# Kernel optimization log

Hardware: AMD Instinct MI355X
Metric: run time of the kernel (lower is better)

The kernel has to match this reference:

```python
import jax, jax.numpy as jnp
import numpy as np

B, T, C, H, N = 2, 1024, 2048, 32, 64
LAYER_ID, N_LAYERS = 12, 24
EPS = 1e-5 * 8 ** 2  # GroupNorm eps = 1e-5 * head_size_divisor**2


def setup_inputs() -> dict:
    key = jax.random.key(0)
    ks = jax.random.split(key, 16)
    nrm = lambda i, shape, s: jax.random.normal(ks[i], shape, jnp.float32) * s
    r01 = LAYER_ID / (N_LAYERS - 1)
    r1a0 = 1.0 - LAYER_ID / N_LAYERS
    ddd = (jnp.arange(C, dtype=jnp.float32) / C)[None, None, :]
    nn_ = jnp.arange(C, dtype=jnp.float32) / (C - 1)
    decay_speed = -7.0 + 5.0 * nn_ ** (0.85 + r01 ** 0.5)
    lin_s = 1.0 / float(np.sqrt(C))
    inp = dict(
        x=nrm(0, (B, T, C), 1.0),
        v_first=nrm(1, (B, T, C), 1.0),
        shift_state=jnp.zeros((B, C), jnp.float32),
        wkv_state=jnp.zeros((B, H, N, N), jnp.float32),
        x_r=1.0 - ddd ** (0.2 * r1a0),
        x_w=1.0 - ddd ** (0.9 * r1a0),
        x_k=1.0 - (ddd ** (0.9 * r1a0) + 0.4 * r01),
        x_v=1.0 - (ddd ** (0.4 * r1a0) + 0.6 * r01),
        x_a=1.0 - ddd ** (0.9 * r1a0),
        x_g=1.0 - ddd ** (0.2 * r1a0),
        w0=decay_speed[None, None, :] + 0.5,
        w1=nrm(2, (C, 64), 0.05), w2=nrm(3, (64, C), 0.1),
        a0=jnp.zeros((1, 1, C), jnp.float32),
        a1=nrm(4, (C, 64), 0.05), a2=nrm(5, (64, C), 0.1),
        v0=jnp.ones((1, 1, C), jnp.float32),
        v1=nrm(6, (C, 32), 0.05), v2=nrm(7, (32, C), 0.1),
        g1=nrm(8, (C, 128), 0.05), g2=nrm(9, (128, C), 0.1),
        k_k=jnp.full((1, 1, C), 0.85, jnp.float32),
        k_a=jnp.ones((1, 1, C), jnp.float32),
        r_k=nrm(10, (H, N), 0.02),
        W_r=nrm(11, (C, C), lin_s), W_k=nrm(12, (C, C), lin_s),
        W_v=nrm(13, (C, C), lin_s), W_o=nrm(14, (C, C), lin_s),
        ln_w=jnp.ones((C,), jnp.float32), ln_b=jnp.zeros((C,), jnp.float32),
    )
    return inp


def _forward(x, v_first, shift_state, wkv_state, x_r, x_w, x_k, x_v, x_a, x_g,
             w0, w1, w2, a0, a1, a2, v0, v1, v2, g1, g2, k_k, k_a, r_k,
             W_r, W_k, W_v, W_o, ln_w, ln_b):
    # token shift
    xx = jnp.concatenate([shift_state[:, None, :], x[:, :-1]], axis=1) - x
    xr, xw, xk, xv, xa, xg = (x + xx * m for m in (x_r, x_w, x_k, x_v, x_a, x_g))
    r = xr @ W_r
    k = xk @ W_k
    v = xv @ W_v
    # log-decay (strictly negative)
    w_log = -jax.nn.softplus(-(w0 + jnp.tanh(xw @ w1) @ w2)) - 0.5
    # residual value mixing towards layer-0 v (layer_id > 0 branch)
    v = v + (v_first - v) * jax.nn.sigmoid(v0 + xv @ v1 @ v2)
    a = jax.nn.sigmoid(a0 + xa @ a1 @ a2)
    g = jax.nn.sigmoid(xg @ g1) @ g2
    # per-head L2-normalized removal key
    kk = (k * k_k).reshape(B, T, H, N)
    kk = kk / jnp.maximum(jnp.linalg.norm(kk, axis=-1, keepdims=True), 1e-12)
    k2 = k * (1.0 + (a - 1.0) * k_a)
    # time-major [T,B,H,N] for the scan
    tm = lambda t: t.reshape(B, T, H, N).transpose(1, 0, 2, 3)
    rs, ks_, vs = tm(r), tm(k2), tm(v)
    ws = jnp.exp(tm(w_log))               # per-channel decay in (0,1)
    a_in = -kk.transpose(1, 0, 2, 3)      # removal direction
    b_in = (kk * a.reshape(B, T, H, N)).transpose(1, 0, 2, 3)
    def step(S, t):  # S: [B,H,Nv,Nk]
        r_, k_, v_, w_, a_, b_ = t
        sa = jnp.einsum('bhvk,bhk->bhv', S, a_)
        S = S * w_[:, :, None, :] \
            + jnp.einsum('bhv,bhk->bhvk', sa, b_) \
            + jnp.einsum('bhv,bhk->bhvk', v_, k_)
        return S, jnp.einsum('bhvk,bhk->bhv', S, r_)
    S_final, o = jax.lax.scan(step, wkv_state, (rs, ks_, vs, ws, a_in, b_in))
    o = o.transpose(1, 0, 2, 3)           # [B,T,H,N]
    # GroupNorm with H groups over C channels (per-head normalization)
    mu = o.mean(-1, keepdims=True)
    var = ((o - mu) ** 2).mean(-1, keepdims=True)
    on = ((o - mu) / jnp.sqrt(var + EPS)).reshape(B, T, C) * ln_w + ln_b
    # rkv bonus term
    rr, kr, vr = r.reshape(B, T, H, N), k2.reshape(B, T, H, N), v.reshape(B, T, H, N)
    bonus = ((rr * kr * r_k).sum(-1, keepdims=True) * vr).reshape(B, T, C)
    out = ((on + bonus) * g) @ W_o
    return out


def reference(x, v_first, shift_state, wkv_state, x_r, x_w, x_k, x_v, x_a, x_g,
              w0, w1, w2, a0, a1, a2, v0, v1, v2, g1, g2, k_k, k_a, r_k,
              W_r, W_k, W_v, W_o, ln_w, ln_b):
    return _forward(x, v_first, shift_state, wkv_state, x_r, x_w, x_k, x_v, x_a, x_g,
                    w0, w1, w2, a0, a1, a2, v0, v1, v2, g1, g2, k_k, k_a, r_k,
                    W_r, W_k, W_v, W_o, ln_w, ln_b)
```

## Files before the change

### kernel.cpp

```cpp
#include <hip/hip_runtime.h>
#include <cstdint>
#include <cstddef>


#define DI __device__ __forceinline__
static constexpr int T_ = 1024, C_ = 2048, H_ = 32;

typedef __attribute__((ext_vector_type(8))) __bf16 bf16x8;
typedef __attribute__((ext_vector_type(4))) float f32x4;
typedef __attribute__((ext_vector_type(8))) unsigned short us8v;
typedef __attribute__((ext_vector_type(4))) unsigned short us4v;
typedef __attribute__((ext_vector_type(2))) unsigned short us2v;

DI float sig_(float z) { return 1.0f / (1.0f + expf(-z)); }

DI unsigned short f2bf(float f) {
  union { float f; uint32_t u; } v; v.f = f;
  uint32_t u = v.u;
  return (unsigned short)((u + 0x7FFFu + ((u >> 16) & 1u)) >> 16);
}
DI float bf2f(unsigned short h) {
  union { uint32_t u; float f; } v; v.u = ((uint32_t)h) << 16;
  return v.f;
}

DI float dpp_xor1_add(float x) {
  int r = __builtin_amdgcn_update_dpp(0, __float_as_int(x), 0xB1, 0xF, 0xF, true);
  return x + __int_as_float(r);
}
DI float dpp_xor2_add(float x) {
  int r = __builtin_amdgcn_update_dpp(0, __float_as_int(x), 0x4E, 0xF, 0xF, true);
  return x + __int_as_float(r);
}
DI float dpp_hm_add(float x) {
  int r = __builtin_amdgcn_update_dpp(0, __float_as_int(x), 0x141, 0xF, 0xF, true);
  return x + __int_as_float(r);
}
DI float dpp_mir_add(float x) {
  int r = __builtin_amdgcn_update_dpp(0, __float_as_int(x), 0x140, 0xF, 0xF, true);
  return x + __int_as_float(r);
}

DI void gload16(const float* g, float* l) {
  __builtin_amdgcn_global_load_lds(
      (const __attribute__((address_space(1))) uint32_t*)g,
      (__attribute__((address_space(3))) uint32_t*)l, 16, 0, 0);
}
DI void gload16u(const unsigned short* g, unsigned short* l) {
  __builtin_amdgcn_global_load_lds(
      (const __attribute__((address_space(1))) uint32_t*)g,
      (__attribute__((address_space(3))) uint32_t*)l, 16, 0, 0);
}
DI void gload4(const float* g, float* l) {
  __builtin_amdgcn_global_load_lds(
      (const __attribute__((address_space(1))) uint32_t*)g,
      (__attribute__((address_space(3))) uint32_t*)l, 4, 0, 0);
}

struct TJob { const float* src; unsigned short* dh; unsigned short* dl;
              int N, K, ntn, tile_end; };
struct TJobs { TJob j[12]; };

__global__ __launch_bounds__(256) void wtrans(TJobs P) {
  __shared__ float t[64][65];
  int bx = blockIdx.x, ji = 0;
  while (ji < 11 && bx >= P.j[ji].tile_end) ++ji;
  TJob J = P.j[ji];
  int tix = bx - (ji ? P.j[ji - 1].tile_end : 0);
  int kt = tix / J.ntn, nt = tix % J.ntn;
  int k0 = kt * 64, n0 = nt * 64;
  int tid = threadIdx.x;
  #pragma unroll
  for (int p = 0; p < 16; ++p) {
    int flat = p * 256 + tid;
    int r = flat >> 6, c = flat & 63;
    int n = n0 + c;
    t[r][c] = (n < J.N && k0 + r < J.K) ? J.src[(size_t)(k0 + r) * J.N + n] : 0.0f;
  }
  __syncthreads();
  #pragma unroll
  for (int p = 0; p < 8; ++p) {
    int flat = p * 256 + tid;
    int rr = flat >> 5, cc = (flat & 31) * 2;
    if (n0 + rr < J.N && k0 + cc < J.K) {
      float w0v = t[cc][rr], w1v = t[cc + 1][rr];
      unsigned short h0 = f2bf(w0v), h1 = f2bf(w1v);
      us2v oh, ol;
      oh.x = h0; oh.y = h1;
      ol.x = f2bf(w0v - bf2f(h0));
      ol.y = f2bf(w1v - bf2f(h1));
      size_t off = (size_t)(n0 + rr) * J.K + k0 + cc;
      *(us2v*)(J.dh + off) = oh;
      *(us2v*)(J.dl + off) = ol;
    }
  }
}

struct GJob {
  const float* A; const unsigned short* Wh; const unsigned short* Wl; float* C;
  const float* mixv; const float* shift; const float* bias;
  int N, K, ntn, kbeg, kend, atomicC, aact, epi, tile_end;
};
struct GJobs { GJob j[8]; };

__global__ __launch_bounds__(256, 2) void gemm_w256(GJobs P) {
  __shared__ unsigned short Ash[128][32];
  __shared__ unsigned short Asl[128][32];
  __shared__ unsigned short Bsh[256][32];
  __shared__ unsigned short Bsl[256][32];
  int bx = blockIdx.x, ji = 0;
  while (ji < 7 && bx >= P.j[ji].tile_end) ++ji;
  GJob J = P.j[ji];
  int tix = bx - (ji ? P.j[ji - 1].tile_end : 0);
  int mt = tix / J.ntn, nt = tix % J.ntn;
  int m0 = mt * 128, n0 = nt * 256;
  int tid = threadIdx.x;
  int lane = tid & 63, wid = tid >> 6;
  int wr = wid >> 1, wc = wid & 1;
  int l15 = lane & 15, lg = lane >> 4;
  f32x4 acc[4][8] = {};

  int sr4 = tid >> 2, sk8 = (tid & 3) * 8;
  float ax[2][8], aq[2][8], amv[8];

  auto loadA = [&](int k0) {
    int kk = k0 + sk8;
    if (J.mixv) {
      *(float4*)&amv[0] = *(const float4*)(J.mixv + kk);
      *(float4*)&amv[4] = *(const float4*)(J.mixv + kk + 4);
    }
    #pragma unroll
    for (int p = 0; p < 2; ++p) {
      int m = m0 + p * 64 + sr4;
      const float* xp0 = J.A + (size_t)m * J.K + kk;
      *(float4*)&ax[p][0] = *(const float4*)xp0;
      *(float4*)&ax[p][4] = *(const float4*)(xp0 + 4);
      if (J.mixv) {
        const float* pp = ((m & (T_ - 1)) == 0)
            ? (J.shift + (size_t)(m >> 10) * C_ + kk)
            : (xp0 - C_);
        *(float4*)&aq[p][0] = *(const float4*)pp;
        *(float4*)&aq[p][4] = *(const float4*)(pp + 4);
      }
    }
  };
  auto writeA = [&]() {
    #pragma unroll
    for (int p = 0; p < 2; ++p) {
      int r = p * 64 + sr4;
      us8v oh, ol;
      #pragma unroll
      for (int q = 0; q < 8; ++q) {
        float va = ax[p][q];
        if (J.mixv) va = va + (aq[p][q] - va) * amv[q];
        if (J.aact == 1) va = tanhf(va);
        else if (J.aact == 2) va = sig_(va);
        unsigned short hq = f2bf(va);
        oh[q] = hq;
        ol[q] = f2bf(va - bf2f(hq));
      }
      int sp = ((tid & 3) ^ ((r >> 1) & 3)) * 8;
      *(us8v*)&Ash[r][sp] = oh;
      *(us8v*)&Asl[r][sp] = ol;
    }
  };
  auto stageB = [&](int k0) {
    #pragma unroll
    for (int j = 0; j < 4; ++j) {
      int r0 = wid * 64 + j * 16;
      int rdst = r0 + (lane >> 2);
      int nrow = n0 + rdst;
      if (nrow >= J.N) nrow = J.N - 1;
      int ssrc = (lane & 3) ^ ((rdst >> 1) & 3);
      size_t gofs = (size_t)nrow * J.K + k0 + ssrc * 8;
      gload16u(J.Wh + gofs, &Bsh[r0][0]);
      gload16u(J.Wl + gofs, &Bsl[r0][0]);
    }
  };

  loadA(J.kbeg);
  stageB(J.kbeg);
  writeA();
  asm volatile("s_waitcnt vmcnt(0)" ::: "memory");
  __syncthreads();

  for (int k0 = J.kbeg; k0 < J.kend; k0 += 32) {
    bool more = (k0 + 32 < J.kend);
    if (more) loadA(k0 + 32);
    bf16x8 afh[4], afl[4];
    #pragma unroll
    for (int i = 0; i < 4; ++i) {
      int rr = wr * 64 + i * 16 + l15;
      int sa_ = (lg ^ ((rr >> 1) & 3)) * 8;
      afh[i] = __builtin_bit_cast(bf16x8, *(const us8v*)&Ash[rr][sa_]);
      afl[i] = __builtin_bit_cast(bf16x8, *(const us8v*)&Asl[rr][sa_]);
    }
    #pragma unroll
    for (int jn = 0; jn < 8; ++jn) {
      int rb = wc * 128 + jn * 16 + l15;
      int sl = (lg ^ ((rb >> 1) & 3)) * 8;
      bf16x8 bh = __builtin_bit_cast(bf16x8, *(const us8v*)&Bsh[rb][sl]);
      bf16x8 bl = __builtin_bit_cast(bf16x8, *(const us8v*)&Bsl[rb][sl]);
      #pragma unroll
      for (int i = 0; i < 4; ++i) {
        acc[i][jn] = __builtin_amdgcn_mfma_f32_16x16x32_bf16(afh[i], bh, acc[i][jn], 0, 0, 0);
        acc[i][jn] = __builtin_amdgcn_mfma_f32_16x16x32_bf16(afl[i], bh, acc[i][jn], 0, 0, 0);
        acc[i][jn] = __builtin_amdgcn_mfma_f32_16x16x32_bf16(afh[i], bl, acc[i][jn], 0, 0, 0);
      }
    }
    __syncthreads();
    if (more) { stageB(k0 + 32); writeA(); }
    asm volatile("s_waitcnt vmcnt(0)" ::: "memory");
    __syncthreads();
  }

  int orow0 = m0 + wr * 64 + 4 * lg;
  int ocol0 = n0 + wc * 128 + l15;
  #pragma unroll
  for (int i = 0; i < 4; ++i) {
    #pragma unroll
    for (int jn = 0; jn < 8; ++jn) {
      int col = ocol0 + jn * 16;
      if (col < J.N) {
        #pragma unroll
        for (int rr = 0; rr < 4; ++rr) {
          size_t idx = (size_t)(orow0 + i * 16 + rr) * J.N + col;
          float v = acc[i][jn][rr];
          if (J.epi == 1) v = sig_(J.bias[col] + v);
          else if (J.epi == 2) v = 0.60653065971263342f * sig_(J.bias[col] + v);
          if (J.atomicC)          atomicAdd(&J.C[idx], v);
          else if (J.epi == 3)    ((unsigned short*)J.C)[idx] = f2bf(v);
          else                    J.C[idx] = v;
        }
      }
    }
  }
}

__global__ __launch_bounds__(256) void prescan(
    float* __restrict__ kio, float* __restrict__ vio,
    float* __restrict__ amat_ain, float* __restrict__ vmix_bin,
    const float* __restrict__ vfirst,
    const float* __restrict__ k_k, const float* __restrict__ k_a) {
  int gh = blockIdx.x * 4 + (threadIdx.x >> 6);
  int lane = threadIdx.x & 63;
  int h = gh & (H_ - 1);
  size_t base = (size_t)gh * 64 + lane;
  int cc = h * 64 + lane;
  float kv = kio[base];
  float kkv = kv * k_k[cc];
  float ss = kkv * kkv;
  ss += __shfl_xor(ss, 1);  ss += __shfl_xor(ss, 2);  ss += __shfl_xor(ss, 4);
  ss += __shfl_xor(ss, 8);  ss += __shfl_xor(ss, 16); ss += __shfl_xor(ss, 32);
  float nrm = fmaxf(sqrtf(ss), 1e-12f);
  float kkn = kkv / nrm;
  float av = amat_ain[base];
  float vmv = vmix_bin[base];
  float vv = vio[base];
  kio[base] = kv * (1.0f + (av - 1.0f) * k_a[cc]);
  vio[base] = vv + (vfirst[base] - vv) * vmv;
  amat_ain[base] = -kkn;
  vmix_bin[base] = kkn * av;
}

static constexpr int CH = 8;
static constexpr int SEG = 512, WU = 96;

#define LOADSTEP(BUF, S_, Aa, Ww, Kk, Bb, Rr, Vt)                  \
  {                                                                \
    *(float4*)&Aa[0] = *(const float4*)&lds[BUF][3][S_][kb];       \
    *(float4*)&Ww[0] = *(const float4*)&lds[BUF][2][S_][kb];       \
    *(float4*)&Kk[0] = *(const float4*)&lds[BUF][1][S_][kb];       \
    *(float4*)&Bb[0] = *(const float4*)&lds[BUF][4][S_][kb];       \
    *(float4*)&Rr[0] = *(const float4*)&lds[BUF][0][S_][kb];       \
    Vt = vtl[BUF][S_][vr];                                         \
  }

#define COMPSTEP(Aa, Ww, Kk, Bb, Rr, Vt, TIDX)                              \
  {                                                                         \
    float p0 = S[0] * Aa[0], p1 = S[1] * Aa[1];                             \
    p0 = fmaf(S[2], Aa[2], p0);                                             \
    p1 = fmaf(S[3], Aa[3], p1);                                             \
    float sa = p0 + p1;                                                     \
    sa = dpp_xor1_add(sa);                                                  \
    sa = dpp_xor2_add(sa);                                                  \
    sa = dpp_hm_add(sa);                                                    \
    sa = dpp_mir_add(sa);                                                   \
    S[0] = fmaf(S[0], Ww[0], fmaf(Vt, Kk[0], sa * Bb[0]));                  \
    S[1] = fmaf(S[1], Ww[1], fmaf(Vt, Kk[1], sa * Bb[1]));                  \
    S[2] = fmaf(S[2], Ww[2], fmaf(Vt, Kk[2], sa * Bb[2]));                  \
    S[3] = fmaf(S[3], Ww[3], fmaf(Vt, Kk[3], sa * Bb[3]));                  \
    float y0 = S[0] * Rr[0], y1 = S[1] * Rr[1];                             \
    y0 = fmaf(S[2], Rr[2], y0);                                             \
    y1 = fmaf(S[3], Rr[3], y1);                                             \
    float y = y0 + y1;                                                      \
    y = dpp_xor1_add(y);                                                    \
    y = dpp_xor2_add(y);                                                    \
    y = dpp_hm_add(y);                                                      \
    y = dpp_mir_add(y);                                                     \
    if (kq == 0 && (TIDX) >= outfrom)                                       \
      obf[bh + (size_t)(TIDX)*2048 + v0 + vr] = f2bf(y);                    \
  }

__global__ __launch_bounds__(128) void wkv_scan_v8(
    const float* __restrict__ r, const float* __restrict__ k2,
    const float* __restrict__ w, const float* __restrict__ ain,
    const float* __restrict__ bin, const float* __restrict__ vp,
    const float* __restrict__ sInit, unsigned short* __restrict__ obf) {
  __shared__ float lds[2][5][CH][64];
  __shared__ float vtl[2][CH][8];
  int D = blockIdx.x;
  int chain = (D & 7) + 8 * (D >> 7);
  int inner = (D >> 3) & 15;
  int seg = inner >> 3, vpair = inner & 7;
  int b = chain >> 5, h = chain & 31;
  int v0 = vpair * 8;
  int tid = threadIdx.x;
  int wid = tid >> 6, lane = tid & 63;
  int vl = lane >> 4, kq = lane & 15;
  int kb = kq * 4;
  int vr = wid * 4 + vl;
  size_t bh = (size_t)(b * T_) * 2048 + (size_t)h * 64;

  float S[4];
  if (seg == 0) {
    const float* sp = sInit + (((size_t)chain * 64 + v0 + vr) * 64) + kb;
    float4 s0 = *(const float4*)sp;
    S[0] = s0.x; S[1] = s0.y; S[2] = s0.z; S[3] = s0.w;
  } else {
    S[0] = S[1] = S[2] = S[3] = 0.0f;
  }

  const float* arr[5] = {r, k2, w, ain, bin};

  auto stage = [&](int buf, int t0) {
    for (int d = wid; d < 10; d += 2) {
      int a = d >> 1, hf = d & 1;
      size_t gofs = bh + (size_t)(t0 + hf * 4 + (lane >> 4)) * 2048 + (lane & 15) * 4;
      gload16(arr[a] + gofs, &lds[buf][a][hf * 4][0]);
    }
    if (wid == 0) {
      size_t gofs = bh + (size_t)(t0 + (lane >> 3)) * 2048 + v0 + (lane & 7);
      gload4(vp + gofs, &vtl[buf][0][0]);
    }
  };

  int tstart = seg ? (SEG - WU) : 0;
  int nch = (seg ? (SEG + WU) : SEG) / CH;
  int outfrom = seg * SEG;

  stage(0, tstart);
  asm volatile("s_waitcnt vmcnt(0)" ::: "memory");
  __syncthreads();

  float A0[4], W0[4], K0[4], B0[4], R0[4], vt0;
  float A1[4], W1[4], K1[4], B1[4], R1[4], vt1;

  for (int c = 0; c < nch; ++c) {
    int cur = c & 1;
    int t0 = tstart + c * CH;
    if (c + 1 < nch) stage(cur ^ 1, t0 + CH);
    LOADSTEP(cur, 0, A0, W0, K0, B0, R0, vt0);
    #pragma unroll 2
    for (int s = 0; s < CH; s += 2) {
      LOADSTEP(cur, s + 1, A1, W1, K1, B1, R1, vt1);
      COMPSTEP(A0, W0, K0, B0, R0, vt0, t0 + s);
      if (s + 2 < CH) LOADSTEP(cur, s + 2, A0, W0, K0, B0, R0, vt0);
      COMPSTEP(A1, W1, K1, B1, R1, vt1, t0 + s + 1);
    }
    asm volatile("s_waitcnt vmcnt(0)" ::: "memory");
    __syncthreads();
  }
}

__global__ __launch_bounds__(256) void post(
    const unsigned short* __restrict__ obf, const float* __restrict__ r,
    const float* __restrict__ k2, const float* __restrict__ vp,
    const unsigned short* __restrict__ gbf, const float* __restrict__ r_k,
    const float* __restrict__ lnw, const float* __restrict__ lnb,
    float* __restrict__ afin) {
  int gh = blockIdx.x * 4 + (threadIdx.x >> 6);
  int lane = threadIdx.x & 63;
  int h = gh & 31;
  size_t base = (size_t)gh * 64 + lane;
  int cc = h * 64 + lane;
  float ov = bf2f(obf[base]);
  float pr = r[base] * k2[base] * r_k[cc];
  float so = ov, so2 = ov * ov, sd = pr;
  #pragma unroll
  for (int d = 1; d <= 32; d <<= 1) {
    so  += __shfl_xor(so, d);
    so2 += __shfl_xor(so2, d);
    sd  += __shfl_xor(sd, d);
  }
  float mu = so * (1.0f / 64.0f);
  float var = so2 * (1.0f / 64.0f) - mu * mu;
  float on = (ov - mu) * rsqrtf(var + 6.4e-4f) * lnw[cc] + lnb[cc];
  float val = (on + sd * vp[base]) * bf2f(gbf[base]);
  afin[base] = val;
}

static constexpr size_t KB = 1024;
static constexpr size_t O_R    = 0;
static constexpr size_t O_K    = 16384;
static constexpr size_t O_V    = 32768;
static constexpr size_t O_WDEC = 49152;
static constexpr size_t O_AMAT = 65536;
static constexpr size_t O_VMIX = 81920;
static constexpr size_t O_AIN  = O_AMAT;
static constexpr size_t O_BIN  = O_VMIX;
static constexpr size_t O_AFIN = O_VMIX;
static constexpr size_t O_WRT_H = 49152, O_WRT_L = 57344;
static constexpr size_t O_WKT_H = 65536, O_WKT_L = 73728;
static constexpr size_t O_WVT_H = 81920, O_WVT_L = 90112;
static constexpr size_t O_W1T_H = 98304, O_W1T_L = 98560;
static constexpr size_t O_A1T_H = 98816, O_A1T_L = 99072;
static constexpr size_t O_V1T_H = 99328, O_V1T_L = 99456;
static constexpr size_t O_G1T_H = 99584, O_G1T_L = 100096;
static constexpr size_t O_WOT_H = 0, O_WOT_L = 8192;
static constexpr size_t D_W2T_H = 10496, D_W2T_L = 10752;
static constexpr size_t D_A2T_H = 11008, D_A2T_L = 11264;
static constexpr size_t D_V2T_H = 11520, D_V2T_L = 11648;
static constexpr size_t D_G2T_H = 11776, D_G2T_L = 12288;

extern "C" void kernel_launch(void* const* d_in, const int* in_sizes, int n_in,
                              void* d_out, int out_size, void* d_ws, size_t ws_size,
                              hipStream_t stream) {
  const float* x      = (const float*)d_in[0];
  const float* vfirst = (const float*)d_in[1];
  const float* shift  = (const float*)d_in[2];
  const float* wkv0   = (const float*)d_in[3];
  const float* x_r = (const float*)d_in[4];
  const float* x_w = (const float*)d_in[5];
  const float* x_k = (const float*)d_in[6];
  const float* x_v = (const float*)d_in[7];
  const float* x_a = (const float*)d_in[8];
  const float* x_g = (const float*)d_in[9];
  const float* w0 = (const float*)d_in[10];
  const float* w1 = (const float*)d_in[11];
  const float* w2 = (const float*)d_in[12];
  const float* a0 = (const float*)d_in[13];
  const float* a1 = (const float*)d_in[14];
  const float* a2 = (const float*)d_in[15];
  const float* v0 = (const float*)d_in[16];
  const float* v1 = (const float*)d_in[17];
  const float* v2 = (const float*)d_in[18];
  const float* g1 = (const float*)d_in[19];
  const float* g2 = (const float*)d_in[20];
  const float* k_k = (const float*)d_in[21];
  const float* k_a = (const float*)d_in[22];
  const float* r_k = (const float*)d_in[23];
  const float* W_r = (const float*)d_in[24];
  const float* W_k = (const float*)d_in[25];
  const float* W_v = (const float*)d_in[26];
  const float* W_o = (const float*)d_in[27];
  const float* ln_w = (const float*)d_in[28];
  const float* ln_b = (const float*)d_in[29];

  char* ws = (char*)d_ws;
  auto F = [&](size_t kb) { return (float*)(ws + kb * KB); };
  auto U = [&](size_t kb) { return (unsigned short*)(ws + kb * KB); };
  auto D = [&](size_t kb) { return (unsigned short*)((char*)d_out + kb * KB); };
  float* outp = (float*)d_out;
  unsigned short* gbf = (unsigned short*)d_out;
  unsigned short* obf = (unsigned short*)((char*)d_out + 8192 * KB);
  float* HW2 = (float*)((char*)d_out + 8192 * KB);
  float* HA2 = (float*)((char*)d_out + 8704 * KB);
  float* HV2 = (float*)((char*)d_out + 9216 * KB);
  float* HG2 = (float*)((char*)d_out + 9472 * KB);

  {
    TJobs TG{};
    int cum = 0, i = 0;
    auto addT = [&](const float* src, unsigned short* dh, unsigned short* dl,
                    int N, int K) {
      int ntn = (N + 63) / 64;
      cum += ((K + 63) / 64) * ntn;
      TG.j[i++] = TJob{src, dh, dl, N, K, ntn, cum};
    };
    addT(W_r, U(O_WRT_H), U(O_WRT_L), 2048, 2048);
    addT(W_k, U(O_WKT_H), U(O_WKT_L), 2048, 2048);
    addT(W_v, U(O_WVT_H), U(O_WVT_L), 2048, 2048);
    addT(w1, U(O_W1T_H), U(O_W1T_L), 64, 2048);
    addT(a1, U(O_A1T_H), U(O_A1T_L), 64, 2048);
    addT(v1, U(O_V1T_H), U(O_V1T_L), 32, 2048);
    addT(g1, U(O_G1T_H), U(O_G1T_L), 128, 2048);
    addT(w2, D(D_W2T_H), D(D_W2T_L), 2048, 64);
    addT(a2, D(D_A2T_H), D(D_A2T_L), 2048, 64);
    addT(v2, D(D_V2T_H), D(D_V2T_L), 2048, 32);
    addT(g2, D(D_G2T_H), D(D_G2T_L), 2048, 128);
    wtrans<<<dim3(cum), dim3(256), 0, stream>>>(TG);
  }

  {
    GJobs G{};
    int cum = 0, i = 0;
    auto add = [&](size_t hkb, size_t lkb, float* Cp, const float* mixv, int N) {
      int ntn = (N + 255) / 256;
      cum += 16 * ntn;
      G.j[i++] = GJob{x, U(hkb), U(lkb), Cp, mixv, shift, nullptr,
                      N, 2048, ntn, 0, 2048, 0, 0, 0, cum};
    };
    add(O_WRT_H, O_WRT_L, F(O_R), x_r, 2048);
    add(O_WKT_H, O_WKT_L, F(O_K), x_k, 2048);
    add(O_WVT_H, O_WVT_L, F(O_V), x_v, 2048);
    add(O_W1T_H, O_W1T_L, HW2, x_w, 64);
    add(O_A1T_H, O_A1T_L, HA2, x_a, 64);
    add(O_V1T_H, O_V1T_L, HV2, x_v, 32);
    add(O_G1T_H, O_G1T_L, HG2, x_g, 128);
    gemm_w256<<<dim3(cum), dim3(256), 0, stream>>>(G);
  }

  {
    GJobs G{};
    int cum = 0, i = 0;
    auto add = [&](const float* A, size_t whkb, size_t wlkb, float* Cp,
                   const float* bias, int K, int aact, int epi) {
      cum += 16 * 8;
      G.j[i++] = GJob{A, D(whkb), D(wlkb), Cp, nullptr, nullptr, bias,
                      2048, K, 8, 0, K, 0, aact, epi, cum};
    };
    add(HW2, D_W2T_H, D_W2T_L, F(O_WDEC), w0, 64, 1, 2);
    add(HA2, D_A2T_H, D_A2T_L, F(O_AMAT), a0, 64, 0, 1);
    add(HV2, D_V2T_H, D_V2T_L, F(O_VMIX), v0, 32, 0, 1);
    add(HG2, D_G2T_H, D_G2T_L, (float*)gbf, nullptr, 128, 2, 3);
    gemm_w256<<<dim3(cum), dim3(256), 0, stream>>>(G);
  }

  prescan<<<dim3(16384), dim3(256), 0, stream>>>(F(O_K), F(O_V), F(O_AMAT), F(O_VMIX),
                                                 vfirst, k_k, k_a);

  wkv_scan_v8<<<dim3(1024), dim3(128), 0, stream>>>(F(O_R), F(O_K), F(O_WDEC), F(O_AIN),
                                                    F(O_BIN), F(O_V), wkv0, obf);

  post<<<dim3(16384), dim3(256), 0, stream>>>(obf, F(O_R), F(O_K), F(O_V),
                                              gbf, r_k, ln_w, ln_b, F(O_AFIN));

  hipMemsetAsync(d_out, 0, (size_t)16384 * KB, stream);

  {
    TJobs TO{};
    TO.j[0] = TJob{W_o, U(O_WOT_H), U(O_WOT_L), 2048, 2048, 32, 1024};
    wtrans<<<dim3(1024), dim3(256), 0, stream>>>(TO);
  }

  {
    GJobs G{};
    G.j[0] = GJob{F(O_AFIN), U(O_WOT_H), U(O_WOT_L), outp, nullptr, nullptr, nullptr,
                  2048, 2048, 8, 0, 1024, 1, 0, 0, 128};
    G.j[1] = GJob{F(O_AFIN), U(O_WOT_H), U(O_WOT_L), outp, nullptr, nullptr, nullptr,
                  2048, 2048, 8, 1024, 2048, 1, 0, 0, 256};
    gemm_w256<<<dim3(256), dim3(256), 0, stream>>>(G);
  }

  (void)in_sizes; (void)n_in; (void)out_size; (void)ws_size;
}
```

Baseline: 827.9 us.

## Coalesce A-tile loads with padded LDS and split output GEMM K four ways

The A-tile staging now has each thread load one float4 across four row groups instead of two float4s across two, so eight consecutive threads cover a contiguous 128-byte row segment. The XOR swizzle on the A shared tile is replaced by padding rows to 40 elements to avoid bank conflicts. Separately, the final W_o GEMM is split-K four ways instead of two, doubling the grid to 512 blocks to fill more CUs, at the cost of more atomic adds on the output and slightly more LDS per block.

```diff
diff --git a/kernel.cpp b/kernel.cpp
--- a/kernel.cpp
+++ b/kernel.cpp
@@ -104,8 +104,8 @@
 struct GJobs { GJob j[8]; };
 
 __global__ __launch_bounds__(256, 2) void gemm_w256(GJobs P) {
-  __shared__ unsigned short Ash[128][32];
-  __shared__ unsigned short Asl[128][32];
+  __shared__ unsigned short Ash[128][40];
+  __shared__ unsigned short Asl[128][40];
   __shared__ unsigned short Bsh[256][32];
   __shared__ unsigned short Bsl[256][32];
   int bx = blockIdx.x, ji = 0;
@@ -120,37 +120,31 @@
   int l15 = lane & 15, lg = lane >> 4;
   f32x4 acc[4][8] = {};
 
-  int sr4 = tid >> 2, sk8 = (tid & 3) * 8;
-  float ax[2][8], aq[2][8], amv[8];
+  int sr = tid >> 3, skq = tid & 7;
+  float ax[4][4], aq[4][4], amv[4];
 
   auto loadA = [&](int k0) {
-    int kk = k0 + sk8;
-    if (J.mixv) {
-      *(float4*)&amv[0] = *(const float4*)(J.mixv + kk);
-      *(float4*)&amv[4] = *(const float4*)(J.mixv + kk + 4);
-    }
+    int kk = k0 + skq * 4;
+    if (J.mixv) *(float4*)amv = *(const float4*)(J.mixv + kk);
     #pragma unroll
-    for (int p = 0; p < 2; ++p) {
-      int m = m0 + p * 64 + sr4;
+    for (int p = 0; p < 4; ++p) {
+      int m = m0 + p * 32 + sr;
       const float* xp0 = J.A + (size_t)m * J.K + kk;
-      *(float4*)&ax[p][0] = *(const float4*)xp0;
-      *(float4*)&ax[p][4] = *(const float4*)(xp0 + 4);
+      *(float4*)ax[p] = *(const float4*)xp0;
       if (J.mixv) {
         const float* pp = ((m & (T_ - 1)) == 0)
             ? (J.shift + (size_t)(m >> 10) * C_ + kk)
             : (xp0 - C_);
-        *(float4*)&aq[p][0] = *(const float4*)pp;
-        *(float4*)&aq[p][4] = *(const float4*)(pp + 4);
+        *(float4*)aq[p] = *(const float4*)pp;
       }
     }
   };
   auto writeA = [&]() {
     #pragma unroll
-    for (int p = 0; p < 2; ++p) {
-      int r = p * 64 + sr4;
-      us8v oh, ol;
+    for (int p = 0; p < 4; ++p) {
+      us4v oh, ol;
       #pragma unroll
-      for (int q = 0; q < 8; ++q) {
+      for (int q = 0; q < 4; ++q) {
         float va = ax[p][q];
         if (J.mixv) va = va + (aq[p][q] - va) * amv[q];
         if (J.aact == 1) va = tanhf(va);
@@ -159,9 +153,9 @@
         oh[q] = hq;
         ol[q] = f2bf(va - bf2f(hq));
       }
-      int sp = ((tid & 3) ^ ((r >> 1) & 3)) * 8;
-      *(us8v*)&Ash[r][sp] = oh;
-      *(us8v*)&Asl[r][sp] = ol;
+      int r = p * 32 + sr;
+      *(us4v*)&Ash[r][skq * 4] = oh;
+      *(us4v*)&Asl[r][skq * 4] = ol;
     }
   };
   auto stageB = [&](int k0) {
@@ -191,9 +185,8 @@
     #pragma unroll
     for (int i = 0; i < 4; ++i) {
       int rr = wr * 64 + i * 16 + l15;
-      int sa_ = (lg ^ ((rr >> 1) & 3)) * 8;
-      afh[i] = __builtin_bit_cast(bf16x8, *(const us8v*)&Ash[rr][sa_]);
-      afl[i] = __builtin_bit_cast(bf16x8, *(const us8v*)&Asl[rr][sa_]);
+      afh[i] = __builtin_bit_cast(bf16x8, *(const us8v*)&Ash[rr][lg * 8]);
+      afl[i] = __builtin_bit_cast(bf16x8, *(const us8v*)&Asl[rr][lg * 8]);
     }
     #pragma unroll
     for (int jn = 0; jn < 8; ++jn) {
@@ -547,10 +540,14 @@
   {
     GJobs G{};
     G.j[0] = GJob{F(O_AFIN), U(O_WOT_H), U(O_WOT_L), outp, nullptr, nullptr, nullptr,
-                  2048, 2048, 8, 0, 1024, 1, 0, 0, 128};
+                  2048, 2048, 8, 0, 512, 1, 0, 0, 128};
     G.j[1] = GJob{F(O_AFIN), U(O_WOT_H), U(O_WOT_L), outp, nullptr, nullptr, nullptr,
-                  2048, 2048, 8, 1024, 2048, 1, 0, 0, 256};
-    gemm_w256<<<dim3(256), dim3(256), 0, stream>>>(G);
+                  2048, 2048, 8, 512, 1024, 1, 0, 0, 256};
+    G.j[2] = GJob{F(O_AFIN), U(O_WOT_H), U(O_WOT_L), outp, nullptr, nullptr, nullptr,
+                  2048, 2048, 8, 1024, 1536, 1, 0, 0, 384};
+    G.j[3] = GJob{F(O_AFIN), U(O_WOT_H), U(O_WOT_L), outp, nullptr, nullptr, nullptr,
+                  2048, 2048, 8, 1536, 2048, 1, 0, 0, 512};
+    gemm_w256<<<dim3(512), dim3(256), 0, stream>>>(G);
   }
 
   (void)in_sizes; (void)n_in; (void)out_size; (void)ws_size;
```

Result: no change. 830.0 us (+0.3%).
